# Performance work log

Measured on AMD Instinct MI355X. Metric: run time of the kernel, lower is better.

## Reference

```python
import jax, jax.numpy as jnp
import numpy as np

B, T, E, H = 8, 2048, 1024, 128


def setup_inputs() -> dict:
    key = jax.random.key(0)
    kx, kk, kq, kv = jax.random.split(key, 4)
    x = jax.random.normal(kx, (B, T, E), dtype=jnp.float32)
    # nn.Linear(E, H, bias=False) weights, stored as (E, H) so y = x @ W
    scale = 0.02
    Wk = jax.random.normal(kk, (E, H), dtype=jnp.float32) * scale
    Wq = jax.random.normal(kq, (E, H), dtype=jnp.float32) * scale
    Wv = jax.random.normal(kv, (E, H), dtype=jnp.float32) * scale
    return {"x": x, "Wk": Wk, "Wq": Wq, "Wv": Wv}


def reference(x, Wk, Wq, Wv):
    # x: (B,T,E) -> k,q,v: (B,T,H)
    k = x @ Wk
    q = x @ Wq
    v = x @ Wv
    # att[b,t,s] = q[b,t] . k[b,s]
    att = jnp.einsum('bth,bsh->bts', q, k)
    # original: att / head_norm, head_norm = 1/sqrt(H)  => multiply by sqrt(H)
    att = att * jnp.sqrt(jnp.float32(H))
    tril = jnp.tril(jnp.ones((T, T), dtype=bool))
    att = jnp.where(tril, att, -jnp.inf)
    # original softmax over dim=1 (query axis), NOT the key axis
    att = jax.nn.softmax(att, axis=1)
    return att @ v  # (B,T,H)
```

## Files before the change

### kernel.cpp

```cpp
#include <hip/hip_runtime.h>
#include <math.h>

#define Bn 8
#define Tn 2048
#define En 1024
#define Hn 128
#define SQRTH 11.313708498984761f

typedef __attribute__((ext_vector_type(8))) short short8;
typedef __attribute__((ext_vector_type(4))) short short4v;
typedef __attribute__((ext_vector_type(4))) float float4v;

#define MFMA16(a, b, c) __builtin_amdgcn_mfma_f32_16x16x32_bf16((a), (b), (c), 0, 0, 0)

static __device__ __forceinline__ unsigned short f2bf(float f) {
    unsigned u = __float_as_uint(f);
    u += 0x7FFFu + ((u >> 16) & 1u);
    return (unsigned short)(u >> 16);
}
static __device__ __forceinline__ float bf2f(unsigned short h) {
    return __uint_as_float(((unsigned)h) << 16);
}

static __device__ __forceinline__ void gll16(const unsigned short* g, unsigned short* l) {
    __builtin_amdgcn_global_load_lds(
        (const __attribute__((address_space(1))) unsigned int*)g,
        (__attribute__((address_space(3))) unsigned int*)l, 16, 0, 0);
}


__global__ __launch_bounds__(256) void wtrans_kernel(
    const float* __restrict__ Wq, const float* __restrict__ Wk, const float* __restrict__ Wv,
    unsigned short* __restrict__ wtt_hi, unsigned short* __restrict__ wtt_lo)
{
    int t = blockIdx.x * 256 + threadIdx.x;
    int kc8 = t & 3;
    int hh = (t >> 2) & 127;
    int ks = (t >> 9) & 31;
    int z = t >> 14;
    const float* W = (z == 0) ? Wq : ((z == 1) ? Wk : Wv);
    short8 h8, l8;
#pragma unroll
    for (int j = 0; j < 8; j++) {
        int e = ks * 32 + kc8 * 8 + j;
        float v = W[(size_t)e * Hn + hh];
        unsigned short hi = f2bf(v);
        h8[j] = (short)hi;
        l8[j] = (short)f2bf(v - bf2f(hi));
    }
    size_t d = (((size_t)z * 32 + ks) * 4096) + (size_t)hh * 32
             + (size_t)(kc8 ^ (hh & 3)) * 8;
    *(short8*)(wtt_hi + d) = h8;
    *(short8*)(wtt_lo + d) = l8;
}

__global__ __launch_bounds__(256) void xconv_kernel(
    const float* __restrict__ x,
    unsigned short* __restrict__ xt_hi, unsigned short* __restrict__ xt_lo)
{
    int g = blockIdx.x * 256 + threadIdx.x;
    int kc8 = g & 3;
    int rr = (g >> 2) & 63;
    int ks = (g >> 8) & 31;
    int mt = g >> 13;
    size_t src = ((size_t)mt * 64 + rr) * En + ks * 32 + kc8 * 8;
    float4v f0 = *(const float4v*)(x + src);
    float4v f1 = *(const float4v*)(x + src + 4);
    short8 h, l;
#pragma unroll
    for (int j = 0; j < 4; j++) {
        unsigned short h0 = f2bf(f0[j]);
        h[j] = (short)h0; l[j] = (short)f2bf(f0[j] - bf2f(h0));
        unsigned short h1 = f2bf(f1[j]);
        h[j + 4] = (short)h1; l[j + 4] = (short)f2bf(f1[j] - bf2f(h1));
    }
    size_t d = (size_t)(g >> 2) * 32 + (size_t)(kc8 ^ (rr & 3)) * 8;
    *(short8*)(xt_hi + d) = h;
    *(short8*)(xt_lo + d) = l;
}

__global__ __launch_bounds__(256) void proj_kernel(
    const unsigned short* __restrict__ xt_hi, const unsigned short* __restrict__ xt_lo,
    const unsigned short* __restrict__ wtt_hi, const unsigned short* __restrict__ wtt_lo,
    unsigned short* __restrict__ q_hi, unsigned short* __restrict__ q_lo,
    unsigned short* __restrict__ k_hi, unsigned short* __restrict__ k_lo,
    unsigned short* __restrict__ vtt)
{
    __shared__ __align__(16) unsigned short lds[2][12288];
    int z = blockIdx.y;
    int mt = blockIdx.x;
    int tid = threadIdx.x;
    int wave = tid >> 6, lane = tid & 63;
    int c15 = lane & 15, kg = lane >> 4;
    int sb = c15 & 3;
    int mrow = wave >> 1, ncol = wave & 1;

    const unsigned short* Ah0 = xt_hi + (size_t)mt * 32 * 2048;
    const unsigned short* Al0 = xt_lo + (size_t)mt * 32 * 2048;
    const unsigned short* Bh0 = wtt_hi + (size_t)z * 32 * 4096;
    const unsigned short* Bl0 = wtt_lo + (size_t)z * 32 * 4096;

    float4v acc[2][4];
#pragma unroll
    for (int i = 0; i < 2; i++)
#pragma unroll
        for (int j = 0; j < 4; j++) acc[i][j] = (float4v)0.0f;

    const unsigned short* gcur[6];
    int lbo[6];
    int gstep[6];
    if (z < 2) {
#pragma unroll
        for (int i = 0; i < 6; i++) {
            int ch = wave * 6 + i;
            if (ch < 4)       { gcur[i] = Ah0 + ch * 512;        lbo[i] = ch * 512;               gstep[i] = 2048; }
            else if (ch < 8)  { gcur[i] = Al0 + (ch - 4) * 512;  lbo[i] = 2048 + (ch - 4) * 512;  gstep[i] = 2048; }
            else if (ch < 16) { gcur[i] = Bh0 + (ch - 8) * 512;  lbo[i] = 4096 + (ch - 8) * 512;  gstep[i] = 4096; }
            else              { gcur[i] = Bl0 + (ch - 16) * 512; lbo[i] = 8192 + (ch - 16) * 512; gstep[i] = 4096; }
        }
    } else {
#pragma unroll
        for (int i = 0; i < 3; i++) {
            int ch = wave * 3 + i;
            if (ch < 4) { gcur[i] = Ah0 + ch * 512;       lbo[i] = ch * 512;              gstep[i] = 2048; }
            else        { gcur[i] = Bh0 + (ch - 4) * 512; lbo[i] = 4096 + (ch - 4) * 512; gstep[i] = 4096; }
        }
    }
    int lo8 = lane * 8;

    auto stage = [&](int buf) {
        unsigned short* Lb = lds[0] + buf * 12288;
        if (z < 2) {
#pragma unroll
            for (int i = 0; i < 6; i++) {
                gll16(gcur[i] + lo8, Lb + lbo[i] + lo8);
                gcur[i] += gstep[i];
            }
        } else {
#pragma unroll
            for (int i = 0; i < 3; i++) {
                gll16(gcur[i] + lo8, Lb + lbo[i] + lo8);
                gcur[i] += gstep[i];
            }
        }
    };

    stage(0);

    for (int ks = 0; ks < 32; ks++) {
        __syncthreads();
        if (ks + 1 < 32) stage((ks + 1) & 1);
        const unsigned short* Lb = lds[ks & 1];

        short8 ah[2], al[2], bh[4], bl[4];
#pragma unroll
        for (int mi = 0; mi < 2; mi++) {
            int row = mrow * 32 + mi * 16 + c15;
            ah[mi] = *(const short8*)(Lb + row * 32 + (kg ^ sb) * 8);
        }
#pragma unroll
        for (int ni = 0; ni < 4; ni++) {
            int row = ncol * 64 + ni * 16 + c15;
            bh[ni] = *(const short8*)(Lb + 4096 + row * 32 + (kg ^ sb) * 8);
        }
        if (z < 2) {
#pragma unroll
            for (int mi = 0; mi < 2; mi++) {
                int row = mrow * 32 + mi * 16 + c15;
                al[mi] = *(const short8*)(Lb + 2048 + row * 32 + (kg ^ sb) * 8);
            }
#pragma unroll
            for (int ni = 0; ni < 4; ni++) {
                int row = ncol * 64 + ni * 16 + c15;
                bl[ni] = *(const short8*)(Lb + 8192 + row * 32 + (kg ^ sb) * 8);
            }
#pragma unroll
            for (int mi = 0; mi < 2; mi++)
#pragma unroll
                for (int ni = 0; ni < 4; ni++) {
                    acc[mi][ni] = MFMA16(ah[mi], bh[ni], acc[mi][ni]);
                    acc[mi][ni] = MFMA16(ah[mi], bl[ni], acc[mi][ni]);
                    acc[mi][ni] = MFMA16(al[mi], bh[ni], acc[mi][ni]);
                }
        } else {
#pragma unroll
            for (int mi = 0; mi < 2; mi++)
#pragma unroll
                for (int ni = 0; ni < 4; ni++)
                    acc[mi][ni] = MFMA16(ah[mi], bh[ni], acc[mi][ni]);
        }
    }

    if (z < 2) {
        unsigned short* oh = (z == 0) ? q_hi : k_hi;
        unsigned short* ol = (z == 0) ? q_lo : k_lo;
#pragma unroll
        for (int mi = 0; mi < 2; mi++) {
#pragma unroll
            for (int ni = 0; ni < 4; ni++) {
                int h = ncol * 64 + ni * 16 + c15;
#pragma unroll
                for (int r = 0; r < 4; r++) {
                    int t = mt * 64 + mrow * 32 + mi * 16 + kg * 4 + r;
                    float v = acc[mi][ni][r];
                    unsigned short hh = f2bf(v);
                    unsigned short ll = f2bf(v - bf2f(hh));
                    size_t o = (size_t)t * Hn + (((h >> 3) ^ (t & 15)) << 3) + (h & 7);
                    oh[o] = hh;
                    ol[o] = ll;
                }
            }
        }
    } else {
        int b = mt >> 5;
#pragma unroll
        for (int mi = 0; mi < 2; mi++) {
            int t0 = (mt & 31) * 64 + mrow * 32 + mi * 16 + kg * 4;
            int sc = t0 >> 5, so = t0 & 31;
#pragma unroll
            for (int ni = 0; ni < 4; ni++) {
                int h = ncol * 64 + ni * 16 + c15;
                short4v pk;
#pragma unroll
                for (int r = 0; r < 4; r++) pk[r] = (short)f2bf(acc[mi][ni][r]);
                int so2 = ((((so >> 3) ^ ((h >> 1) & 3))) << 3) | (so & 7);
                *(short4v*)(vtt + (((size_t)b * 64 + sc) * 128 + h) * 32 + so2) = pk;
            }
        }
    }
}

__global__ __launch_bounds__(256) void stats_part_kernel(
    const unsigned short* __restrict__ q_hi, const unsigned short* __restrict__ q_lo,
    const unsigned short* __restrict__ k_hi, const unsigned short* __restrict__ k_lo,
    float* __restrict__ m_part, float* __restrict__ l_part)
{
    __shared__ __align__(16) unsigned short lds[8192];
    int tid = threadIdx.x;
    int wave = tid >> 6, lane = tid & 63;
    int c15 = lane & 15, kg = lane >> 4;
    int b = blockIdx.x;

    int rem = (int)blockIdx.y, sj, nch = 1;
    for (sj = 0; sj < 32; sj++) {
        nch = ((31 - sj) >> 2) + 1;
        if (rem < nch) break;
        rem -= nch;
    }
    int ci = rem;
    int c0 = 2 * sj;
    int len = 64 - c0;
    int cbase = len / nch, ext = len % nch;
    int cs = c0 + ci * cbase + (ci < ext ? ci : ext);
    int ce = cs + cbase + (ci < ext ? 1 : 0);

    int s_base = sj * 64 + wave * 16;

    short8 a_h[4], a_l[4];
    {
        int s = s_base + c15;
        const unsigned short* kr = k_hi + ((size_t)(b * Tn + s)) * Hn;
        const unsigned short* krl = k_lo + ((size_t)(b * Tn + s)) * Hn;
#pragma unroll
        for (int st = 0; st < 4; st++) {
            int off = ((st * 4 + kg) ^ c15) * 8;
            a_h[st] = *(const short8*)(kr + off);
            a_l[st] = *(const short8*)(krl + off);
        }
    }
    float m[4], l[4];
#pragma unroll
    for (int r = 0; r < 4; r++) { m[r] = -3.0e38f; l[r] = 0.0f; }

    auto stage = [&](int c) {
        const unsigned short* Qh = q_hi + ((size_t)b * Tn + c * 32) * Hn;
        const unsigned short* Ql = q_lo + ((size_t)b * Tn + c * 32) * Hn;
        int lo8 = lane * 8;
#pragma unroll
        for (int i = 0; i < 4; i++) {
            int ch = wave * 4 + i;
            const unsigned short* g;
            unsigned short* ld;
            if (ch < 8) { g = Qh + ch * 512;       ld = lds + ch * 512; }
            else        { g = Ql + (ch - 8) * 512; ld = lds + 4096 + (ch - 8) * 512; }
            gll16(g + lo8, ld + lo8);
        }
    };

    for (int c = cs; c < ce; c++) {
        stage(c);
        __syncthreads();
#pragma unroll
        for (int half = 0; half < 2; half++) {
            int t16 = c * 32 + half * 16;
            int tl = half * 16 + c15;
            float4v a1 = (float4v)0.0f, a2 = (float4v)0.0f, a3 = (float4v)0.0f;
#pragma unroll
            for (int st = 0; st < 4; st++) {
                int off = tl * 128 + ((st * 4 + kg) ^ c15) * 8;
                short8 bh = *(const short8*)(lds + off);
                short8 bl = *(const short8*)(lds + 4096 + off);
                a1 = MFMA16(a_h[st], bh, a1);
                a2 = MFMA16(a_h[st], bl, a2);
                a3 = MFMA16(a_l[st], bh, a3);
            }
            int t = t16 + c15;
#pragma unroll
            for (int r = 0; r < 4; r++) {
                float attv = (a1[r] + a2[r] + a3[r]) * SQRTH;
                int s_row = s_base + kg * 4 + r;
                bool valid = (t >= s_row);
                float cand = valid ? attv : -3.0e38f;
                float mn = fmaxf(m[r], cand);
                l[r] = l[r] * __expf(m[r] - mn) + (valid ? __expf(attv - mn) : 0.0f);
                m[r] = mn;
            }
        }
        __syncthreads();
    }
#pragma unroll
    for (int mask = 1; mask < 16; mask <<= 1) {
#pragma unroll
        for (int r = 0; r < 4; r++) {
            float mo = __shfl_xor(m[r], mask);
            float lo2 = __shfl_xor(l[r], mask);
            float mn = fmaxf(m[r], mo);
            l[r] = l[r] * __expf(m[r] - mn) + lo2 * __expf(mo - mn);
            m[r] = mn;
        }
    }
    if (c15 == 0) {
#pragma unroll
        for (int r = 0; r < 4; r++) {
            int sl = wave * 16 + kg * 4 + r;
            size_t d = ((((size_t)b * 32 + sj) * 8 + ci) * 64) + sl;
            m_part[d] = m[r];
            l_part[d] = l[r];
        }
    }
}

__global__ __launch_bounds__(256) void stats_combine_kernel(
    const float* __restrict__ m_part, const float* __restrict__ l_part,
    float* __restrict__ m_st, float* __restrict__ il_st)
{
    int g = blockIdx.x * 256 + threadIdx.x;
    int s = g & 2047, b = g >> 11;
    int sj = s >> 6, sl = s & 63;
    int nch = ((31 - sj) >> 2) + 1;
    size_t base = (((size_t)b * 32 + sj) * 8) * 64 + sl;
    float M = m_part[base];
    float L = l_part[base];
    for (int ci = 1; ci < nch; ci++) {
        float mi = m_part[base + (size_t)ci * 64];
        float li = l_part[base + (size_t)ci * 64];
        float mn = fmaxf(M, mi);
        L = L * __expf(M - mn) + li * __expf(mi - mn);
        M = mn;
    }
    m_st[(size_t)b * Tn + s] = M;
    il_st[(size_t)b * Tn + s] = 1.0f / L;
}

__global__ __launch_bounds__(256) void out_part_kernel(
    const unsigned short* __restrict__ q_hi, const unsigned short* __restrict__ q_lo,
    const unsigned short* __restrict__ k_hi, const unsigned short* __restrict__ k_lo,
    const unsigned short* __restrict__ vtt,
    const float* __restrict__ m_st, const float* __restrict__ il_st,
    float* __restrict__ part_out)
{
    __shared__ __align__(16) unsigned short lds[12288];
    __shared__ __align__(16) unsigned short pbuf[4][16][40];
    int tid = threadIdx.x;
    int wave = tid >> 6, lane = tid & 63;
    int c15 = lane & 15, kg = lane >> 4;
    int b = blockIdx.x;

    int rem = (int)blockIdx.y, tj, nch = 1;
    for (tj = 31; tj >= 0; tj--) {
        nch = (tj >> 2) + 1;
        if (rem < nch) break;
        rem -= nch;
    }
    int ci = rem;
    int len = 2 * tj + 2;
    int cbase = len / nch, ext = len % nch;
    int cs = ci * cbase + (ci < ext ? ci : ext);
    int ce = cs + cbase + (ci < ext ? 1 : 0);

    int t_base = tj * 64 + wave * 16;

    short8 qa_h[4], qa_l[4];
    {
        int t = t_base + c15;
        const unsigned short* qr = q_hi + ((size_t)(b * Tn + t)) * Hn;
        const unsigned short* qrl = q_lo + ((size_t)(b * Tn + t)) * Hn;
#pragma unroll
        for (int st = 0; st < 4; st++) {
            int off = ((st * 4 + kg) ^ c15) * 8;
            qa_h[st] = *(const short8*)(qr + off);
            qa_l[st] = *(const short8*)(qrl + off);
        }
    }
    float4v oacc[8];
#pragma unroll
    for (int i = 0; i < 8; i++) oacc[i] = (float4v)0.0f;

    auto stage = [&](int c) {
        const unsigned short* Kh = k_hi + ((size_t)b * Tn + c * 32) * Hn;
        const unsigned short* Kl = k_lo + ((size_t)b * Tn + c * 32) * Hn;
        const unsigned short* Vv = vtt + ((size_t)b * 64 + c) * (128 * 32);
        int lo8 = lane * 8;
#pragma unroll
        for (int i = 0; i < 6; i++) {
            int ch = wave * 6 + i;
            const unsigned short* g;
            unsigned short* ld;
            if (ch < 8)       { g = Kh + ch * 512;        ld = lds + ch * 512; }
            else if (ch < 16) { g = Kl + (ch - 8) * 512;  ld = lds + 4096 + (ch - 8) * 512; }
            else              { g = Vv + (ch - 16) * 512; ld = lds + 8192 + (ch - 16) * 512; }
            gll16(g + lo8, ld + lo8);
        }
    };

    for (int c = cs; c < ce; c++) {
        stage(c);
        __syncthreads();
#pragma unroll
        for (int half = 0; half < 2; half++) {
            int s16 = c * 32 + half * 16;
            int sl = half * 16 + c15;
            float4v a1 = (float4v)0.0f, a2 = (float4v)0.0f, a3 = (float4v)0.0f;
#pragma unroll
            for (int st = 0; st < 4; st++) {
                int off = sl * 128 + ((st * 4 + kg) ^ c15) * 8;
                short8 bh = *(const short8*)(lds + off);
                short8 bl = *(const short8*)(lds + 4096 + off);
                a1 = MFMA16(qa_h[st], bh, a1);
                a2 = MFMA16(qa_h[st], bl, a2);
                a3 = MFMA16(qa_l[st], bh, a3);
            }
            float msv = m_st[b * Tn + s16 + c15];
            float ilv = il_st[b * Tn + s16 + c15];
#pragma unroll
            for (int r = 0; r < 4; r++) {
                int t = t_base + kg * 4 + r;
                float attv = (a1[r] + a2[r] + a3[r]) * SQRTH;
                float earg = fminf(attv - msv, 0.0f);
                float p = (t >= s16 + c15) ? __expf(earg) * ilv : 0.0f;
                pbuf[wave][kg * 4 + r][c15 + half * 16] = f2bf(p);
            }
        }
        short8 pa = *(const short8*)&pbuf[wave][c15][kg * 8];
#pragma unroll
        for (int nt = 0; nt < 8; nt++) {
            int voff = (nt * 16 + c15) * 32 + ((kg ^ ((c15 >> 1) & 3)) * 8);
            short8 vb = *(const short8*)(lds + 8192 + voff);
            oacc[nt] = MFMA16(pa, vb, oacc[nt]);
        }
        __syncthreads();
    }
    float* po = part_out + ((((size_t)b * 32 + tj) * 8 + ci) * 64) * 128;
#pragma unroll
    for (int nt = 0; nt < 8; nt++) {
        int h = nt * 16 + c15;
#pragma unroll
        for (int r = 0; r < 4; r++) {
            int tl = wave * 16 + kg * 4 + r;
            po[(size_t)tl * 128 + h] = oacc[nt][r];
        }
    }
}

__global__ __launch_bounds__(256) void out_combine_kernel(
    const float* __restrict__ part_out, float* __restrict__ out)
{
    int g = blockIdx.x * 256 + threadIdx.x;
    int h4 = g & 31;
    int t = (g >> 5) & 2047;
    int b = g >> 16;
    int tj = t >> 6, tl = t & 63;
    int nch = (tj >> 2) + 1;
    const float4v* p = (const float4v*)(part_out
        + ((((size_t)b * 32 + tj) * 8) * 64 + tl) * 128) + h4;
    float4v acc = p[0];
    for (int ci = 1; ci < nch; ci++) acc += p[(size_t)ci * 2048];
    *((float4v*)(out + ((size_t)b * Tn + t) * Hn) + h4) = acc;
}

extern "C" void kernel_launch(void* const* d_in, const int* in_sizes, int n_in,
                              void* d_out, int out_size, void* d_ws, size_t ws_size,
                              hipStream_t stream)
{
    (void)in_sizes; (void)n_in; (void)out_size; (void)ws_size;
    const float* x  = (const float*)d_in[0];
    const float* Wk = (const float*)d_in[1];
    const float* Wq = (const float*)d_in[2];
    const float* Wv = (const float*)d_in[3];
    float* out = (float*)d_out;

    const size_t NQ = (size_t)Bn * Tn * Hn;
    const size_t NX = (size_t)Bn * Tn * En;
    unsigned short* q_hi = (unsigned short*)d_ws;
    unsigned short* q_lo = q_hi + NQ;
    unsigned short* k_hi = q_lo + NQ;
    unsigned short* k_lo = k_hi + NQ;
    unsigned short* vtt  = k_lo + NQ;
    unsigned short* xt_hi = vtt + NQ;
    unsigned short* xt_lo = xt_hi + NX;
    unsigned short* wtt_hi = xt_lo + NX;
    unsigned short* wtt_lo = wtt_hi + (size_t)3 * Hn * En;
    float* m_st  = (float*)(wtt_lo + (size_t)3 * Hn * En);
    float* il_st = m_st + (size_t)Bn * Tn;

    float* part_out = (float*)xt_hi;
    float* m_part   = (float*)wtt_hi;
    float* l_part   = (float*)wtt_lo;

    wtrans_kernel<<<dim3(192), 256, 0, stream>>>(Wq, Wk, Wv, wtt_hi, wtt_lo);
    xconv_kernel<<<dim3(8192), 256, 0, stream>>>(x, xt_hi, xt_lo);
    proj_kernel<<<dim3(256, 3), 256, 0, stream>>>(xt_hi, xt_lo, wtt_hi, wtt_lo,
                                                  q_hi, q_lo, k_hi, k_lo, vtt);
    stats_part_kernel<<<dim3(Bn, 144), 256, 0, stream>>>(q_hi, q_lo, k_hi, k_lo,
                                                         m_part, l_part);
    stats_combine_kernel<<<dim3(64), 256, 0, stream>>>(m_part, l_part, m_st, il_st);
    out_part_kernel<<<dim3(Bn, 144), 256, 0, stream>>>(q_hi, q_lo, k_hi, k_lo, vtt,
                                                       m_st, il_st, part_out);
    out_combine_kernel<<<dim3(2048), 256, 0, stream>>>(part_out, out);
}
```

Baseline: 208.7 us.

## Double attention row tile to 128 rows with 512-thread blocks in stats and output kernels

Result: slower. 222.3 us (+6.5%).

```diff
diff --git a/kernel.cpp b/kernel.cpp
--- a/kernel.cpp
+++ b/kernel.cpp
@@ -230,7 +230,7 @@
     }
 }
 
-__global__ __launch_bounds__(256) void stats_part_kernel(
+__global__ __launch_bounds__(512) void stats_part_kernel(
     const unsigned short* __restrict__ q_hi, const unsigned short* __restrict__ q_lo,
     const unsigned short* __restrict__ k_hi, const unsigned short* __restrict__ k_lo,
     float* __restrict__ m_part, float* __restrict__ l_part)
@@ -241,20 +241,20 @@
     int c15 = lane & 15, kg = lane >> 4;
     int b = blockIdx.x;
 
-    int rem = (int)blockIdx.y, sj, nch = 1;
-    for (sj = 0; sj < 32; sj++) {
-        nch = ((31 - sj) >> 2) + 1;
+    int rem = (int)blockIdx.y, sj2, nch = 1;
+    for (sj2 = 0; sj2 < 16; sj2++) {
+        nch = ((64 - 4 * sj2) + 7) >> 3;
         if (rem < nch) break;
         rem -= nch;
     }
     int ci = rem;
-    int c0 = 2 * sj;
+    int c0 = 4 * sj2;
     int len = 64 - c0;
     int cbase = len / nch, ext = len % nch;
     int cs = c0 + ci * cbase + (ci < ext ? ci : ext);
     int ce = cs + cbase + (ci < ext ? 1 : 0);
 
-    int s_base = sj * 64 + wave * 16;
+    int s_base = sj2 * 128 + wave * 16;
 
     short8 a_h[4], a_l[4];
     {
@@ -277,8 +277,8 @@
         const unsigned short* Ql = q_lo + ((size_t)b * Tn + c * 32) * Hn;
         int lo8 = lane * 8;
 #pragma unroll
-        for (int i = 0; i < 4; i++) {
-            int ch = wave * 4 + i;
+        for (int i = 0; i < 2; i++) {
+            int ch = wave * 2 + i;
             const unsigned short* g;
             unsigned short* ld;
             if (ch < 8) { g = Qh + ch * 512;       ld = lds + ch * 512; }
@@ -333,7 +333,7 @@
 #pragma unroll
         for (int r = 0; r < 4; r++) {
             int sl = wave * 16 + kg * 4 + r;
-            size_t d = ((((size_t)b * 32 + sj) * 8 + ci) * 64) + sl;
+            size_t d = ((((size_t)b * 16 + sj2) * 8 + ci) * 128) + sl;
             m_part[d] = m[r];
             l_part[d] = l[r];
         }
@@ -346,14 +346,14 @@
 {
     int g = blockIdx.x * 256 + threadIdx.x;
     int s = g & 2047, b = g >> 11;
-    int sj = s >> 6, sl = s & 63;
-    int nch = ((31 - sj) >> 2) + 1;
-    size_t base = (((size_t)b * 32 + sj) * 8) * 64 + sl;
+    int sj2 = s >> 7, sl = s & 127;
+    int nch = ((64 - 4 * sj2) + 7) >> 3;
+    size_t base = (((size_t)b * 16 + sj2) * 8) * 128 + sl;
     float M = m_part[base];
     float L = l_part[base];
     for (int ci = 1; ci < nch; ci++) {
-        float mi = m_part[base + (size_t)ci * 64];
-        float li = l_part[base + (size_t)ci * 64];
+        float mi = m_part[base + (size_t)ci * 128];
+        float li = l_part[base + (size_t)ci * 128];
         float mn = fmaxf(M, mi);
         L = L * __expf(M - mn) + li * __expf(mi - mn);
         M = mn;
@@ -362,7 +362,7 @@
     il_st[(size_t)b * Tn + s] = 1.0f / L;
 }
 
-__global__ __launch_bounds__(256) void out_part_kernel(
+__global__ __launch_bounds__(512) void out_part_kernel(
     const unsigned short* __restrict__ q_hi, const unsigned short* __restrict__ q_lo,
     const unsigned short* __restrict__ k_hi, const unsigned short* __restrict__ k_lo,
     const unsigned short* __restrict__ vtt,
@@ -370,25 +370,25 @@
     float* __restrict__ part_out)
 {
     __shared__ __align__(16) unsigned short lds[12288];
-    __shared__ __align__(16) unsigned short pbuf[4][16][40];
+    __shared__ __align__(16) unsigned short pbuf[8][16][40];
     int tid = threadIdx.x;
     int wave = tid >> 6, lane = tid & 63;
     int c15 = lane & 15, kg = lane >> 4;
     int b = blockIdx.x;
 
-    int rem = (int)blockIdx.y, tj, nch = 1;
-    for (tj = 31; tj >= 0; tj--) {
-        nch = (tj >> 2) + 1;
+    int rem = (int)blockIdx.y, tj2, nch = 1;
+    for (tj2 = 15; tj2 >= 0; tj2--) {
+        nch = (tj2 >> 1) + 1;
         if (rem < nch) break;
         rem -= nch;
     }
     int ci = rem;
-    int len = 2 * tj + 2;
+    int len = 4 * tj2 + 4;
     int cbase = len / nch, ext = len % nch;
     int cs = ci * cbase + (ci < ext ? ci : ext);
     int ce = cs + cbase + (ci < ext ? 1 : 0);
 
-    int t_base = tj * 64 + wave * 16;
+    int t_base = tj2 * 128 + wave * 16;
 
     short8 qa_h[4], qa_l[4];
     {
@@ -412,8 +412,8 @@
         const unsigned short* Vv = vtt + ((size_t)b * 64 + c) * (128 * 32);
         int lo8 = lane * 8;
 #pragma unroll
-        for (int i = 0; i < 6; i++) {
-            int ch = wave * 6 + i;
+        for (int i = 0; i < 3; i++) {
+            int ch = wave * 3 + i;
             const unsigned short* g;
             unsigned short* ld;
             if (ch < 8)       { g = Kh + ch * 512;        ld = lds + ch * 512; }
@@ -460,7 +460,7 @@
         }
         __syncthreads();
     }
-    float* po = part_out + ((((size_t)b * 32 + tj) * 8 + ci) * 64) * 128;
+    float* po = part_out + ((((size_t)b * 16 + tj2) * 8 + ci) * 128) * 128;
 #pragma unroll
     for (int nt = 0; nt < 8; nt++) {
         int h = nt * 16 + c15;
@@ -479,12 +479,12 @@
     int h4 = g & 31;
     int t = (g >> 5) & 2047;
     int b = g >> 16;
-    int tj = t >> 6, tl = t & 63;
-    int nch = (tj >> 2) + 1;
+    int tj2 = t >> 7, tl = t & 127;
+    int nch = (tj2 >> 1) + 1;
     const float4v* p = (const float4v*)(part_out
-        + ((((size_t)b * 32 + tj) * 8) * 64 + tl) * 128) + h4;
+        + ((((size_t)b * 16 + tj2) * 8) * 128 + tl) * 128) + h4;
     float4v acc = p[0];
-    for (int ci = 1; ci < nch; ci++) acc += p[(size_t)ci * 2048];
+    for (int ci = 1; ci < nch; ci++) acc += p[(size_t)ci * 4096];
     *((float4v*)(out + ((size_t)b * Tn + t) * Hn) + h4) = acc;
 }
 
@@ -521,10 +521,10 @@
     xconv_kernel<<<dim3(8192), 256, 0, stream>>>(x, xt_hi, xt_lo);
     proj_kernel<<<dim3(256, 3), 256, 0, stream>>>(xt_hi, xt_lo, wtt_hi, wtt_lo,
                                                   q_hi, q_lo, k_hi, k_lo, vtt);
-    stats_part_kernel<<<dim3(Bn, 144), 256, 0, stream>>>(q_hi, q_lo, k_hi, k_lo,
-                                                         m_part, l_part);
+    stats_part_kernel<<<dim3(Bn, 72), 512, 0, stream>>>(q_hi, q_lo, k_hi, k_lo,
+                                                        m_part, l_part);
     stats_combine_kernel<<<dim3(64), 256, 0, stream>>>(m_part, l_part, m_st, il_st);
-    out_part_kernel<<<dim3(Bn, 144), 256, 0, stream>>>(q_hi, q_lo, k_hi, k_lo, vtt,
-                                                       m_st, il_st, part_out);
+    out_part_kernel<<<dim3(Bn, 72), 512, 0, stream>>>(q_hi, q_lo, k_hi, k_lo, vtt,
+                                                      m_st, il_st, part_out);
     out_combine_kernel<<<dim3(2048), 256, 0, stream>>>(part_out, out);
 }
```
